# Kernel tuning notes

Hardware: AMD Instinct MI355X
Metric: run time of the kernel (lower is better)

## Reference

```python
import jax, jax.numpy as jnp
import numpy as np

N_EMBD = 1024
N_HEAD = 16
HEAD_DIM = N_EMBD // N_HEAD


def setup_inputs() -> dict:
    key = jax.random.key(0)
    kx, kq, kk, kv, ko = jax.random.split(key, 5)
    B, T, C = 2, 2048, N_EMBD
    s = 1.0 / np.sqrt(C)
    return {
        "x": jax.random.normal(kx, (B, T, C), dtype=jnp.float32),
        "Wq": jax.random.normal(kq, (C, C), dtype=jnp.float32) * s,
        "Wk": jax.random.normal(kk, (C, C), dtype=jnp.float32) * s,
        "Wv": jax.random.normal(kv, (C, C), dtype=jnp.float32) * s,
        "Wo": jax.random.normal(ko, (C, C), dtype=jnp.float32) * s,
    }


def reference(x, Wq, Wk, Wv, Wo):
    B, T, C = x.shape
    H, D = N_HEAD, HEAD_DIM
    # projections (torch Linear: y = x @ W^T)
    q = (x @ Wq.T).reshape(B, T, H, D).transpose(0, 2, 1, 3)  # [B,H,T,D]
    k = (x @ Wk.T).reshape(B, T, H, D).transpose(0, 2, 1, 3)
    v = (x @ Wv.T).reshape(B, T, H, D).transpose(0, 2, 1, 3)
    scale = 1.0 / np.sqrt(D).astype(np.float32)
    scores = jnp.einsum("bhqd,bhkd->bhqk", q, k) * scale  # [B,H,T,T]
    causal = jnp.tril(jnp.ones((T, T), dtype=bool))
    scores = jnp.where(causal, scores, -jnp.inf)
    attn = jax.nn.softmax(scores, axis=-1)
    y = jnp.einsum("bhqk,bhkd->bhqd", attn, v)  # [B,H,T,D]
    y = y.transpose(0, 2, 1, 3).reshape(B, T, C)
    return y @ Wo.T
```

## Files before the change

### kernel.cpp

```cpp
#include <hip/hip_runtime.h>
#include <hip/hip_bf16.h>
#include <math.h>

#define SEQ   2048
#define CDIM  1024
#define NH    16
#define HD    64

#define K_SCALE 0.1803368801111204f

typedef __attribute__((ext_vector_type(8))) short bf16x8;
typedef __attribute__((ext_vector_type(4))) float f32x4;
typedef __attribute__((ext_vector_type(4))) short short4v;

__device__ __forceinline__ short f2bf(float f) {
  return (short)__builtin_bit_cast(unsigned short, __float2bfloat16(f));
}

__device__ __forceinline__ void glds16(const short* g, short* l) {
  __builtin_amdgcn_global_load_lds(
      (const __attribute__((address_space(1))) unsigned int*)g,
      (__attribute__((address_space(3))) unsigned int*)l, 16, 0, 0);
}

__global__ void cvt_kernel(const float* __restrict__ src, short* __restrict__ dst, int n4) {
  int i = blockIdx.x * blockDim.x + threadIdx.x;
  if (i >= n4) return;
  float4 v = reinterpret_cast<const float4*>(src)[i];
  short4v o;
  o.x = f2bf(v.x); o.y = f2bf(v.y); o.z = f2bf(v.z); o.w = f2bf(v.w);
  reinterpret_cast<short4v*>(dst)[i] = o;
}

__global__ void cvtw_kernel(const float* __restrict__ w0, const float* __restrict__ w1,
                            const float* __restrict__ w2, const float* __restrict__ w3,
                            short* __restrict__ d0, short* __restrict__ d1,
                            short* __restrict__ d2, short* __restrict__ d3) {
  const int y = blockIdx.y;
  const float* src = (y == 0) ? w0 : (y == 1) ? w1 : (y == 2) ? w2 : w3;
  short* dst       = (y == 0) ? d0 : (y == 1) ? d1 : (y == 2) ? d2 : d3;
  const float mult = (y == 1) ? K_SCALE : 1.0f;
  int i = blockIdx.x * blockDim.x + threadIdx.x;
  float4 v = reinterpret_cast<const float4*>(src)[i];
  short4v o;
  o.x = f2bf(v.x * mult); o.y = f2bf(v.y * mult);
  o.z = f2bf(v.z * mult); o.w = f2bf(v.w * mult);
  reinterpret_cast<short4v*>(dst)[i] = o;
}

template<int MODE, int BN>
__global__ __launch_bounds__(256)
void gemm_bt(const short* __restrict__ A,
             const short* __restrict__ W0, const short* __restrict__ W1, const short* __restrict__ W2,
             short* __restrict__ ob0, short* __restrict__ ob1, short* __restrict__ ob2,
             float* __restrict__ of)
{
  constexpr int K = CDIM;
  constexpr int NJF = BN / 32;
  const int z = (MODE == 0) ? blockIdx.z : 0;
  const short* W;
  short* outb = nullptr;
  if (MODE == 0) {
    W    = (z == 0) ? W0  : (z == 1) ? W1  : W2;
    outb = (z == 0) ? ob0 : (z == 1) ? ob1 : ob2;
  } else {
    W = W0;
  }
  const int m0 = blockIdx.y * 128;
  const int n0 = blockIdx.x * BN;

  __shared__ __align__(16) short As[128 * 32];
  __shared__ __align__(16) short Bs[BN * 32];

  const int tid  = threadIdx.x;
  const int lane = tid & 63;
  const int wid  = tid >> 6;
  const int wr   = wid >> 1;
  const int wc   = wid & 1;
  const int rl   = lane & 15;
  const int g    = lane >> 4;

  f32x4 acc[4][NJF];
#pragma unroll
  for (int i = 0; i < 4; ++i)
#pragma unroll
    for (int j = 0; j < NJF; ++j)
      acc[i][j] = (f32x4){0.f, 0.f, 0.f, 0.f};

  const int lrow = lane >> 2;
  const int lcol = (lane & 3) * 8;
  const int arow = wid * 32 + lrow;

  for (int kt = 0; kt < K / 32; ++kt) {
    const int k0 = kt * 32;
    glds16(&A[(size_t)(m0 + arow) * K + k0 + lcol],      &As[(wid * 32) * 32]);
    glds16(&A[(size_t)(m0 + arow + 16) * K + k0 + lcol], &As[(wid * 32 + 16) * 32]);
    if constexpr (BN == 128) {
      glds16(&W[(size_t)(n0 + arow) * K + k0 + lcol],      &Bs[(wid * 32) * 32]);
      glds16(&W[(size_t)(n0 + arow + 16) * K + k0 + lcol], &Bs[(wid * 32 + 16) * 32]);
    } else {
      glds16(&W[(size_t)(n0 + wid * 16 + lrow) * K + k0 + lcol], &Bs[(wid * 16) * 32]);
    }
    __syncthreads();

    bf16x8 af[4], bfr[NJF];
#pragma unroll
    for (int mi = 0; mi < 4; ++mi)
      af[mi] = *(const bf16x8*)&As[(wr * 64 + mi * 16 + rl) * 32 + g * 8];
#pragma unroll
    for (int nj = 0; nj < NJF; ++nj)
      bfr[nj] = *(const bf16x8*)&Bs[(wc * (BN / 2) + nj * 16 + rl) * 32 + g * 8];
#pragma unroll
    for (int mi = 0; mi < 4; ++mi)
#pragma unroll
      for (int nj = 0; nj < NJF; ++nj)
        acc[mi][nj] = __builtin_amdgcn_mfma_f32_16x16x32_bf16(af[mi], bfr[nj], acc[mi][nj], 0, 0, 0);
    __syncthreads();
  }

#pragma unroll
  for (int mi = 0; mi < 4; ++mi) {
#pragma unroll
    for (int nj = 0; nj < NJF; ++nj) {
      const int gmb = m0 + wr * 64 + mi * 16 + g * 4;
      const int gn  = n0 + wc * (BN / 2) + nj * 16 + rl;
      if (MODE == 0 && z == 2) {
        short4v pk;
#pragma unroll
        for (int r = 0; r < 4; ++r) pk[r] = f2bf(acc[mi][nj][r]);
        const int b = gmb >> 11, t = gmb & 2047;
        const int h = gn >> 6,  d = gn & 63;
        *(short4v*)&outb[(((size_t)(b * NH + h)) * HD + d) * SEQ + t] = pk;
      } else {
#pragma unroll
        for (int r = 0; r < 4; ++r) {
          const int gm = gmb + r;
          const float val = acc[mi][nj][r];
          if (MODE == 0) {
            const int b = gm >> 11, t = gm & 2047;
            const int h = gn >> 6,  d = gn & 63;
            outb[(((size_t)(b * NH + h)) * SEQ + t) * HD + d] = f2bf(val);
          } else {
            of[(size_t)gm * CDIM + gn] = val;
          }
        }
      }
    }
  }
}

__global__ __launch_bounds__(256)
void attn_kernel(const short* __restrict__ q, const short* __restrict__ k,
                 const short* __restrict__ vt, short* __restrict__ yb)
{
  const int bh  = blockIdx.y;
  const int pp  = blockIdx.x;
  const int jA  = pp;
  const int jB  = 31 - pp;
  const int tid = threadIdx.x;
  const int lane = tid & 63;
  const int wid  = tid >> 6;
  const int rl   = lane & 15;
  const int g    = lane >> 4;

  const short* Qp = q  + (size_t)bh * SEQ * HD;
  const short* Kp = k  + (size_t)bh * SEQ * HD;
  const short* Vp = vt + (size_t)bh * HD * SEQ;

  __shared__ short Ks[64 * 72];
  __shared__ short Vs[64 * 72];
  __shared__ short Ps[4][2][16 * 72];

  const int q0A = jA * 64 + wid * 16;
  const int q0B = jB * 64 + wid * 16;

  bf16x8 qfA[2], qfB[2];
#pragma unroll
  for (int ds = 0; ds < 2; ++ds) {
    qfA[ds] = *(const bf16x8*)&Qp[(size_t)(q0A + rl) * HD + ds * 32 + g * 8];
    qfB[ds] = *(const bf16x8*)&Qp[(size_t)(q0B + rl) * HD + ds * 32 + g * 8];
  }

  const short one_bf = (short)0x3F80;
  const bf16x8 onesv = (bf16x8){one_bf, one_bf, one_bf, one_bf,
                                one_bf, one_bf, one_bf, one_bf};

  f32x4 accA[4], accB[4], lAcc, lBcc;
#pragma unroll
  for (int nt = 0; nt < 4; ++nt) { accA[nt] = (f32x4){0,0,0,0}; accB[nt] = (f32x4){0,0,0,0}; }
  lAcc = (f32x4){0,0,0,0}; lBcc = (f32x4){0,0,0,0};

  const int srow = tid >> 3;
  const int scol = (tid & 7) * 8;

  auto process = [&](bf16x8 (&qf)[2], f32x4 (&acc)[4], f32x4& acc_l,
                     bool diag, int t, int q0w, short* PsW) {
    f32x4 s_[4];
#pragma unroll
    for (int ct = 0; ct < 4; ++ct) s_[ct] = (f32x4){0, 0, 0, 0};
    __builtin_amdgcn_s_setprio(1);
#pragma unroll
    for (int ct = 0; ct < 4; ++ct)
#pragma unroll
      for (int ds = 0; ds < 2; ++ds) {
        bf16x8 kf = *(const bf16x8*)&Ks[(ct * 16 + rl) * 72 + ds * 32 + g * 8];
        s_[ct] = __builtin_amdgcn_mfma_f32_16x16x32_bf16(qf[ds], kf, s_[ct], 0, 0, 0);
      }
    __builtin_amdgcn_s_setprio(0);

#pragma unroll
    for (int ct = 0; ct < 4; ++ct) {
      const int c = ct * 16 + rl;
#pragma unroll
      for (int r = 0; r < 4; ++r) {
        float sv = s_[ct][r];
        if (diag) {
          const int key = t * 64 + ct * 16 + rl;
          const int qq  = q0w + g * 4 + r;
          sv = (key <= qq) ? sv : -INFINITY;
        }
        const float p = exp2f(sv);
        PsW[(g * 4 + r) * 72 + c] = f2bf(p);
      }
    }

    __builtin_amdgcn_s_setprio(1);
#pragma unroll
    for (int ks = 0; ks < 2; ++ks) {
      bf16x8 pf = *(const bf16x8*)&PsW[rl * 72 + ks * 32 + g * 8];
      acc_l = __builtin_amdgcn_mfma_f32_16x16x32_bf16(pf, onesv, acc_l, 0, 0, 0);
#pragma unroll
      for (int nt = 0; nt < 4; ++nt) {
        bf16x8 vf = *(const bf16x8*)&Vs[(nt * 16 + rl) * 72 + ks * 32 + g * 8];
        acc[nt] = __builtin_amdgcn_mfma_f32_16x16x32_bf16(pf, vf, acc[nt], 0, 0, 0);
      }
    }
    __builtin_amdgcn_s_setprio(0);
  };

  auto epilogue = [&](f32x4 (&acc)[4], f32x4& acc_l, int q0w) {
    const int b = bh >> 4, h = bh & 15;
#pragma unroll
    for (int r = 0; r < 4; ++r) {
      const float inv = 1.0f / acc_l[r];
      const int qq = q0w + g * 4 + r;
#pragma unroll
      for (int nt = 0; nt < 4; ++nt)
        yb[((size_t)b * SEQ + qq) * CDIM + h * HD + nt * 16 + rl] = f2bf(acc[nt][r] * inv);
    }
  };

  bf16x8 k0 = *(const bf16x8*)&Kp[(size_t)srow * HD + scol];
  bf16x8 k1 = *(const bf16x8*)&Kp[(size_t)(srow + 32) * HD + scol];
  bf16x8 v0 = *(const bf16x8*)&Vp[(size_t)srow * SEQ + scol];
  bf16x8 v1 = *(const bf16x8*)&Vp[(size_t)(srow + 32) * SEQ + scol];

  for (int t = 0; t <= jB; ++t) {
    __syncthreads();
    *(bf16x8*)&Ks[srow * 72 + scol]        = k0;
    *(bf16x8*)&Ks[(srow + 32) * 72 + scol] = k1;
    *(bf16x8*)&Vs[srow * 72 + scol]        = v0;
    *(bf16x8*)&Vs[(srow + 32) * 72 + scol] = v1;
    __syncthreads();

    if (t < jB) {
      const int kn = (t + 1) * 64;
      k0 = *(const bf16x8*)&Kp[(size_t)(kn + srow) * HD + scol];
      k1 = *(const bf16x8*)&Kp[(size_t)(kn + srow + 32) * HD + scol];
      v0 = *(const bf16x8*)&Vp[(size_t)srow * SEQ + kn + scol];
      v1 = *(const bf16x8*)&Vp[(size_t)(srow + 32) * SEQ + kn + scol];
    }

    process(qfB, accB, lBcc, t == jB, t, q0B, &Ps[wid][0][0]);
    if (t <= jA)
      process(qfA, accA, lAcc, t == jA, t, q0A, &Ps[wid][1][0]);
  }

  epilogue(accB, lBcc, q0B);
  epilogue(accA, lAcc, q0A);
}

extern "C" void kernel_launch(void* const* d_in, const int* in_sizes, int n_in,
                              void* d_out, int out_size, void* d_ws, size_t ws_size,
                              hipStream_t stream) {
  const float* x  = (const float*)d_in[0];
  const float* Wq = (const float*)d_in[1];
  const float* Wk = (const float*)d_in[2];
  const float* Wv = (const float*)d_in[3];
  const float* Wo = (const float*)d_in[4];
  float* out = (float*)d_out;

  char* ws = (char*)d_ws;
  short* xb  = (short*)(ws);
  short* Wqb = (short*)(ws + ((size_t)8  << 20));
  short* Wkb = (short*)(ws + ((size_t)10 << 20));
  short* Wvb = (short*)(ws + ((size_t)12 << 20));
  short* Wob = (short*)(ws + ((size_t)14 << 20));
  short* qb  = (short*)(ws + ((size_t)16 << 20));
  short* kbp = (short*)(ws + ((size_t)24 << 20));
  short* vtp = (short*)(ws + ((size_t)32 << 20));
  short* yb  = (short*)(ws + ((size_t)40 << 20));

  cvt_kernel<<<4096, 256, 0, stream>>>(x, xb, 1048576);
  cvtw_kernel<<<dim3(1024, 4), 256, 0, stream>>>(Wq, Wk, Wv, Wo, Wqb, Wkb, Wvb, Wob);

  gemm_bt<0, 128><<<dim3(8, 32, 3), 256, 0, stream>>>(xb, Wqb, Wkb, Wvb, qb, kbp, vtp, nullptr);

  attn_kernel<<<dim3(16, 32), 256, 0, stream>>>(qb, kbp, vtp, yb);

  gemm_bt<1, 64><<<dim3(16, 32, 1), 256, 0, stream>>>(yb, Wob, nullptr, nullptr,
                                                      nullptr, nullptr, nullptr, out);
}
```

Baseline: 119.3 us.

## Switch attention to 32x32 MFMA tiles with per-wave query block split

The attention kernel now uses 32x32x16 bf16 MFMAs instead of 16x16x32. Each wave owns 32 query rows, and waves 0-1 handle the late block jB while waves 2-3 handle the early block jA, instead of every wave processing both blocks. The larger MFMA tile is meant to cut LDS fragment reads per FLOP and instruction count. The trade-off is load imbalance: waves assigned to jA sit idle once t exceeds jA while still hitting the block barriers.

```diff
diff --git a/kernel.cpp b/kernel.cpp
--- a/kernel.cpp
+++ b/kernel.cpp
@@ -11,6 +11,7 @@
 
 typedef __attribute__((ext_vector_type(8))) short bf16x8;
 typedef __attribute__((ext_vector_type(4))) float f32x4;
+typedef __attribute__((ext_vector_type(16))) float f32x16;
 typedef __attribute__((ext_vector_type(4))) short short4v;
 
 __device__ __forceinline__ short f2bf(float f) {
@@ -160,8 +161,8 @@
   const int tid = threadIdx.x;
   const int lane = tid & 63;
   const int wid  = tid >> 6;
-  const int rl   = lane & 15;
-  const int g    = lane >> 4;
+  const int l31  = lane & 31;
+  const int g2   = lane >> 5;
 
   const short* Qp = q  + (size_t)bh * SEQ * HD;
   const short* Kp = k  + (size_t)bh * SEQ * HD;
@@ -169,86 +170,27 @@
 
   __shared__ short Ks[64 * 72];
   __shared__ short Vs[64 * 72];
-  __shared__ short Ps[4][2][16 * 72];
-
-  const int q0A = jA * 64 + wid * 16;
-  const int q0B = jB * 64 + wid * 16;
-
-  bf16x8 qfA[2], qfB[2];
-#pragma unroll
-  for (int ds = 0; ds < 2; ++ds) {
-    qfA[ds] = *(const bf16x8*)&Qp[(size_t)(q0A + rl) * HD + ds * 32 + g * 8];
-    qfB[ds] = *(const bf16x8*)&Qp[(size_t)(q0B + rl) * HD + ds * 32 + g * 8];
-  }
+  __shared__ short Ps[4][32 * 72];
+
+  const int myJ   = (wid < 2) ? jB : jA;
+  const int tLast = myJ;
+  const int q0w   = myJ * 64 + (wid & 1) * 32;
+
+  bf16x8 qf[4];
+#pragma unroll
+  for (int dk = 0; dk < 4; ++dk)
+    qf[dk] = *(const bf16x8*)&Qp[(size_t)(q0w + l31) * HD + dk * 16 + g2 * 8];
 
   const short one_bf = (short)0x3F80;
   const bf16x8 onesv = (bf16x8){one_bf, one_bf, one_bf, one_bf,
                                 one_bf, one_bf, one_bf, one_bf};
 
-  f32x4 accA[4], accB[4], lAcc, lBcc;
-#pragma unroll
-  for (int nt = 0; nt < 4; ++nt) { accA[nt] = (f32x4){0,0,0,0}; accB[nt] = (f32x4){0,0,0,0}; }
-  lAcc = (f32x4){0,0,0,0}; lBcc = (f32x4){0,0,0,0};
+  f32x16 acc0, acc1, lsum;
+#pragma unroll
+  for (int r = 0; r < 16; ++r) { acc0[r] = 0.f; acc1[r] = 0.f; lsum[r] = 0.f; }
 
   const int srow = tid >> 3;
   const int scol = (tid & 7) * 8;
-
-  auto process = [&](bf16x8 (&qf)[2], f32x4 (&acc)[4], f32x4& acc_l,
-                     bool diag, int t, int q0w, short* PsW) {
-    f32x4 s_[4];
-#pragma unroll
-    for (int ct = 0; ct < 4; ++ct) s_[ct] = (f32x4){0, 0, 0, 0};
-    __builtin_amdgcn_s_setprio(1);
-#pragma unroll
-    for (int ct = 0; ct < 4; ++ct)
-#pragma unroll
-      for (int ds = 0; ds < 2; ++ds) {
-        bf16x8 kf = *(const bf16x8*)&Ks[(ct * 16 + rl) * 72 + ds * 32 + g * 8];
-        s_[ct] = __builtin_amdgcn_mfma_f32_16x16x32_bf16(qf[ds], kf, s_[ct], 0, 0, 0);
-      }
-    __builtin_amdgcn_s_setprio(0);
-
-#pragma unroll
-    for (int ct = 0; ct < 4; ++ct) {
-      const int c = ct * 16 + rl;
-#pragma unroll
-      for (int r = 0; r < 4; ++r) {
-        float sv = s_[ct][r];
-        if (diag) {
-          const int key = t * 64 + ct * 16 + rl;
-          const int qq  = q0w + g * 4 + r;
-          sv = (key <= qq) ? sv : -INFINITY;
-        }
-        const float p = exp2f(sv);
-        PsW[(g * 4 + r) * 72 + c] = f2bf(p);
-      }
-    }
-
-    __builtin_amdgcn_s_setprio(1);
-#pragma unroll
-    for (int ks = 0; ks < 2; ++ks) {
-      bf16x8 pf = *(const bf16x8*)&PsW[rl * 72 + ks * 32 + g * 8];
-      acc_l = __builtin_amdgcn_mfma_f32_16x16x32_bf16(pf, onesv, acc_l, 0, 0, 0);
-#pragma unroll
-      for (int nt = 0; nt < 4; ++nt) {
-        bf16x8 vf = *(const bf16x8*)&Vs[(nt * 16 + rl) * 72 + ks * 32 + g * 8];
-        acc[nt] = __builtin_amdgcn_mfma_f32_16x16x32_bf16(pf, vf, acc[nt], 0, 0, 0);
-      }
-    }
-    __builtin_amdgcn_s_setprio(0);
-  };
-
-  auto epilogue = [&](f32x4 (&acc)[4], f32x4& acc_l, int q0w) {
-    const int b = bh >> 4, h = bh & 15;
-#pragma unroll
-    for (int r = 0; r < 4; ++r) {
-      const float inv = 1.0f / acc_l[r];
-      const int qq = q0w + g * 4 + r;
-#pragma unroll
-      for (int nt = 0; nt < 4; ++nt)
-        yb[((size_t)b * SEQ + qq) * CDIM + h * HD + nt * 16 + rl] = f2bf(acc[nt][r] * inv);
-    }
-  };
 
   bf16x8 k0 = *(const bf16x8*)&Kp[(size_t)srow * HD + scol];
   bf16x8 k1 = *(const bf16x8*)&Kp[(size_t)(srow + 32) * HD + scol];
@@ -271,13 +213,64 @@
       v1 = *(const bf16x8*)&Vp[(size_t)(srow + 32) * SEQ + kn + scol];
     }
 
-    process(qfB, accB, lBcc, t == jB, t, q0B, &Ps[wid][0][0]);
-    if (t <= jA)
-      process(qfA, accA, lAcc, t == jA, t, q0A, &Ps[wid][1][0]);
-  }
-
-  epilogue(accB, lBcc, q0B);
-  epilogue(accA, lAcc, q0A);
+    if (t <= tLast) {
+      const bool diag = (t == tLast);
+      short* PsW = &Ps[wid][0];
+
+      f32x16 s0, s1;
+#pragma unroll
+      for (int r = 0; r < 16; ++r) { s0[r] = 0.f; s1[r] = 0.f; }
+      __builtin_amdgcn_s_setprio(1);
+#pragma unroll
+      for (int dk = 0; dk < 4; ++dk) {
+        bf16x8 kf0 = *(const bf16x8*)&Ks[l31 * 72 + dk * 16 + g2 * 8];
+        s0 = __builtin_amdgcn_mfma_f32_32x32x16_bf16(qf[dk], kf0, s0, 0, 0, 0);
+        bf16x8 kf1 = *(const bf16x8*)&Ks[(32 + l31) * 72 + dk * 16 + g2 * 8];
+        s1 = __builtin_amdgcn_mfma_f32_32x32x16_bf16(qf[dk], kf1, s1, 0, 0, 0);
+      }
+      __builtin_amdgcn_s_setprio(0);
+
+#pragma unroll
+      for (int kb = 0; kb < 2; ++kb) {
+#pragma unroll
+        for (int r = 0; r < 16; ++r) {
+          const int row = (r & 3) + 8 * (r >> 2) + 4 * g2;
+          float sv = (kb == 0) ? s0[r] : s1[r];
+          if (diag) {
+            const int key = t * 64 + kb * 32 + l31;
+            const int qq  = q0w + row;
+            sv = (key <= qq) ? sv : -INFINITY;
+          }
+          const float p = exp2f(sv);
+          PsW[row * 72 + kb * 32 + l31] = f2bf(p);
+        }
+      }
+
+      __builtin_amdgcn_s_setprio(1);
+#pragma unroll
+      for (int ks = 0; ks < 4; ++ks) {
+        bf16x8 pf = *(const bf16x8*)&PsW[l31 * 72 + ks * 16 + g2 * 8];
+        lsum = __builtin_amdgcn_mfma_f32_32x32x16_bf16(pf, onesv, lsum, 0, 0, 0);
+        bf16x8 vf0 = *(const bf16x8*)&Vs[l31 * 72 + ks * 16 + g2 * 8];
+        acc0 = __builtin_amdgcn_mfma_f32_32x32x16_bf16(pf, vf0, acc0, 0, 0, 0);
+        bf16x8 vf1 = *(const bf16x8*)&Vs[(32 + l31) * 72 + ks * 16 + g2 * 8];
+        acc1 = __builtin_amdgcn_mfma_f32_32x32x16_bf16(pf, vf1, acc1, 0, 0, 0);
+      }
+      __builtin_amdgcn_s_setprio(0);
+    }
+  }
+
+  {
+    const int b = bh >> 4, h = bh & 15;
+#pragma unroll
+    for (int r = 0; r < 16; ++r) {
+      const int row = (r & 3) + 8 * (r >> 2) + 4 * g2;
+      const int qq  = q0w + row;
+      const float inv = 1.0f / lsum[r];
+      yb[((size_t)b * SEQ + qq) * CDIM + h * HD + l31]      = f2bf(acc0[r] * inv);
+      yb[((size_t)b * SEQ + qq) * CDIM + h * HD + 32 + l31] = f2bf(acc1[r] * inv);
+    }
+  }
 }
 
 extern "C" void kernel_launch(void* const* d_in, const int* in_sizes, int n_in,
```

New measurement: 145.3 us. 1.22x slower.
